# Optimization experiments

Measured on AMD Instinct MI355X. Metric: run time of the kernel, lower is better.

Reference implementation:

```python
import jax, jax.numpy as jnp
import numpy as np

HIDDEN = 1024
HEADS = 16
HEAD = HIDDEN // HEADS


def setup_inputs() -> dict:
    key = jax.random.key(0)
    ks = jax.random.split(key, 6)
    B, T = 2, 2048
    x = jax.random.normal(ks[0], (B, T, HIDDEN), dtype=jnp.float32)
    mask = jnp.ones((T, T), dtype=jnp.float32)
    s = 1.0 / np.sqrt(HIDDEN)
    Wqkv = jax.random.normal(ks[1], (HIDDEN, 3 * HIDDEN), dtype=jnp.float32) * s
    bqkv = jnp.zeros((3 * HIDDEN,), dtype=jnp.float32)
    Wproj = jax.random.normal(ks[2], (HIDDEN, HIDDEN), dtype=jnp.float32) * s
    bproj = jnp.zeros((HIDDEN,), dtype=jnp.float32)
    return {"x": x, "mask": mask, "Wqkv": Wqkv, "bqkv": bqkv,
            "Wproj": Wproj, "bproj": bproj}


def reference(x, mask, Wqkv, bqkv, Wproj, bproj):
    B, T, C = x.shape
    qkv = x @ Wqkv + bqkv                      # [B,T,3C]
    q, k, v = jnp.split(qkv, 3, axis=-1)
    def heads(t):                              # [B,T,C] -> [B,H,T,D]
        return t.reshape(B, T, HEADS, HEAD).transpose(0, 2, 1, 3)
    q, k, v = heads(q), heads(k), heads(v)
    scores = jnp.einsum('bhqd,bhkd->bhqk', q, k) / np.sqrt(HEAD)
    scores = jnp.where(mask == 0, -jnp.inf, scores)
    attn = jax.nn.softmax(scores, axis=-1)
    out = jnp.einsum('bhqk,bhkd->bhqd', attn, v)
    out = out.transpose(0, 2, 1, 3).reshape(B, T, C)
    return out @ Wproj + bproj
```

## Files before the change

kernel.cpp:

```cpp
#include <hip/hip_runtime.h>
#include <stdint.h>

#define HID 1024
#define NH 16
#define HD 64
#define BATCH 2
#define SEQ 2048
#define MR (BATCH*SEQ)
#define NQKV (3*HID)

typedef __attribute__((ext_vector_type(8))) _Float16 h16x8;
typedef __attribute__((ext_vector_type(4))) _Float16 h16x4;
typedef __attribute__((ext_vector_type(2))) __fp16 fp16x2;
typedef __attribute__((ext_vector_type(8))) unsigned short u16x8;
typedef __attribute__((ext_vector_type(4))) float f32x4;

#if __has_builtin(__builtin_amdgcn_exp2f)
#define EXP2(x) __builtin_amdgcn_exp2f(x)
#else
#define EXP2(x) exp2f(x)
#endif

static __device__ __forceinline__ unsigned short f2h(float f) {
  union { _Float16 h; unsigned short u; } v; v.h = (_Float16)f; return v.u;
}
static __device__ __forceinline__ unsigned pk2(float a, float b) {
  union { fp16x2 h; unsigned u; } v;
  v.h = __builtin_amdgcn_cvt_pkrtz(a, b);
  return v.u;
}

typedef const __attribute__((address_space(1))) unsigned int glb_u32;
typedef __attribute__((address_space(3))) unsigned int lds_u32;
static __device__ __forceinline__ void cp16(const void* g, void* l) {
  __builtin_amdgcn_global_load_lds((glb_u32*)g, (lds_u32*)l, 16, 0, 0);
}

#define QSCL (0.125f * 1.44269504f)

__global__ __launch_bounds__(256) void k_prep(const float4* __restrict__ x4,
                                              const float* __restrict__ mask,
                                              const float* __restrict__ Wqkv,
                                              const float* __restrict__ Wproj,
                                              ushort4* __restrict__ xh,
                                              unsigned short* __restrict__ WqT,
                                              unsigned short* __restrict__ WpT,
                                              unsigned long long* __restrict__ mb) {
  __shared__ float tile[32][33];
  int blk = blockIdx.x, tid = threadIdx.x;
  if (blk < 4096) {
    int i = blk * 256 + tid;
    float4 v = x4[i];
    ushort4 h;
    h.x = f2h(v.x); h.y = f2h(v.y); h.z = f2h(v.z); h.w = f2h(v.w);
    xh[i] = h;
  } else if (blk < 8192) {
    const float* src; unsigned short* dst; int C, bx, by;
    if (blk < 7168) { src = Wqkv;  dst = WqT; C = NQKV; int b2 = blk - 4096; bx = b2 % 96; by = b2 / 96; }
    else            { src = Wproj; dst = WpT; C = HID;  int b2 = blk - 7168; bx = b2 & 31; by = b2 >> 5; }
    int tx = tid & 31, ty = tid >> 5;
    int col0 = bx * 32, row0 = by * 32;
    #pragma unroll
    for (int i = 0; i < 32; i += 8)
      tile[ty + i][tx] = src[(size_t)(row0 + ty + i) * C + col0 + tx];
    __syncthreads();
    #pragma unroll
    for (int i = 0; i < 32; i += 8)
      dst[(size_t)(col0 + ty + i) * HID + row0 + tx] = f2h(tile[tx][ty + i]);
  } else {
    int gw = (blk - 8192) * 4 + (tid >> 6);
    int lane = tid & 63;
    float v = mask[(size_t)gw * 64 + lane];
    unsigned long long b = __ballot(v != 0.f);
    if (lane == 0) mb[gw] = b;
  }
}

__global__ __launch_bounds__(256) void k_gemm_qkv(const unsigned short* __restrict__ A,
                                                  const unsigned short* __restrict__ Bt,
                                                  const float* __restrict__ bias,
                                                  unsigned short* __restrict__ Qp,
                                                  unsigned short* __restrict__ Kp,
                                                  unsigned short* __restrict__ Vt) {
  const int K = HID;
  int tid = threadIdx.x;
  int wave = tid >> 6, lane = tid & 63, quad = lane >> 4, l16 = lane & 15;
  int wm = wave >> 1, wn = wave & 1;
  int x7 = l16 & 7;
  int m0 = blockIdx.y * 128, n0 = blockIdx.x * 128;
  __shared__ __align__(16) unsigned short smem[17408];
  unsigned short* As = smem;
  unsigned short* Bs = smem + 8192;
  unsigned short* Lb = smem;
  f32x4 acc[4][4] = {};
  for (int k0 = 0; k0 < K; k0 += 64) {
    __syncthreads();
    #pragma unroll
    for (int i = 0; i < 4; i++) {
      int c = tid + i * 256;
      int r = c >> 3, sc = ((c ^ r) & 7) << 3;
      cp16(&A[(size_t)(m0 + r) * K + k0 + sc], &As[c << 3]);
      cp16(&Bt[(size_t)(n0 + r) * K + k0 + sc], &Bs[c << 3]);
    }
    __syncthreads();
    #pragma unroll
    for (int kc = 0; kc < 2; kc++) {
      h16x8 af[4], bf[4];
      #pragma unroll
      for (int i = 0; i < 4; i++) {
        af[i] = *(const h16x8*)&As[(wm * 64 + i * 16 + l16) * 64 + (((kc * 4 + quad) ^ x7) << 3)];
        bf[i] = *(const h16x8*)&Bs[(wn * 64 + i * 16 + l16) * 64 + (((kc * 4 + quad) ^ x7) << 3)];
      }
      #pragma unroll
      for (int i = 0; i < 4; i++)
        #pragma unroll
        for (int j = 0; j < 4; j++)
          acc[i][j] = __builtin_amdgcn_mfma_f32_16x16x32_f16(af[i], bf[j], acc[i][j], 0, 0, 0);
    }
  }
  int which = n0 >> 10;
  int hbase = (n0 & 1023) >> 6;
  __syncthreads();
  if (which == 2) {
    #pragma unroll
    for (int j = 0; j < 4; j++) {
      int nl = wn * 64 + j * 16 + l16;
      float bv = bias[n0 + nl];
      #pragma unroll
      for (int i = 0; i < 4; i++) {
        int ml = wm * 64 + i * 16 + quad * 4;
        uint2 tt;
        tt.x = pk2(acc[i][j][0] + bv, acc[i][j][1] + bv);
        tt.y = pk2(acc[i][j][2] + bv, acc[i][j][3] + bv);
        *(uint2*)&Lb[nl * 136 + ml] = tt;
      }
    }
  } else {
    float scl = (which == 0) ? QSCL : 1.0f;
    #pragma unroll
    for (int j = 0; j < 4; j++) {
      int nl = wn * 64 + j * 16 + l16;
      float bv = bias[n0 + nl];
      #pragma unroll
      for (int i = 0; i < 4; i++)
        #pragma unroll
        for (int r = 0; r < 4; r++) {
          int ml = wm * 64 + i * 16 + quad * 4 + r;
          Lb[ml * 136 + nl] = f2h((acc[i][j][r] + bv) * scl);
        }
    }
  }
  __syncthreads();
  int b = m0 >> 11, tb = m0 & 2047;
  if (which == 2) {
    #pragma unroll
    for (int p = 0; p < 8; p++) {
      int c = tid + p * 256;
      int rr = c >> 4, cc = c & 15;
      int h = hbase + (rr >> 6), d = rr & 63;
      u16x8 vv = *(const u16x8*)&Lb[rr * 136 + cc * 8];
      *(u16x8*)&Vt[(size_t)(b * NH + h) * (SEQ * HD) + (size_t)d * SEQ + tb + cc * 8] = vv;
    }
  } else {
    unsigned short* dst = (which == 0) ? Qp : Kp;
    #pragma unroll
    for (int p = 0; p < 8; p++) {
      int c = tid + p * 256;
      int rr = c >> 4, cc = c & 15;
      int h = hbase + (cc >> 3), d0 = (cc & 7) << 3;
      u16x8 vv = *(const u16x8*)&Lb[rr * 136 + cc * 8];
      *(u16x8*)&dst[(size_t)(b * NH + h) * (SEQ * HD) + (size_t)(tb + rr) * HD + d0] = vv;
    }
  }
}

__global__ __launch_bounds__(256) void k_attn(const unsigned short* __restrict__ Qp,
                                              const unsigned short* __restrict__ Kp,
                                              const unsigned short* __restrict__ Vt,
                                              const unsigned long long* __restrict__ mb,
                                              unsigned short* __restrict__ AO) {
  int tid = threadIdx.x, wave = tid >> 6, lane = tid & 63, quad = lane >> 4, l16 = lane & 15;
  int bh = blockIdx.y, qbase = blockIdx.x * 128;
  const unsigned short* Qg = Qp + (size_t)bh * (SEQ * HD);
  const unsigned short* Kg = Kp + (size_t)bh * (SEQ * HD);
  const unsigned short* Vg = Vt + (size_t)bh * (SEQ * HD);
  __shared__ __align__(16) unsigned short smem[24576];
  unsigned short* Qs = smem;
  unsigned short* Os = smem;

  #pragma unroll
  for (int i = 0; i < 4; i++) {
    int c = tid + i * 256;
    int row = c >> 3, sc = ((c ^ row) & 7) << 3;
    cp16(&Qg[(size_t)(qbase + row) * HD + sc], &Qs[c << 3]);
  }
  #pragma unroll
  for (int i = 0; i < 2; i++) {
    int c = tid + i * 256;
    int row = c >> 3, sc = ((c ^ row) & 7) << 3;
    cp16(&Kg[(size_t)row * HD + sc], &smem[8192 + (c << 3)]);
    cp16(&Vg[(size_t)row * SEQ + sc], &smem[12288 + (c << 3)]);
  }
  int q0 = qbase + wave * 32 + l16;
  const unsigned long long* mrow0 = mb + (size_t)q0 * 32;
  const unsigned long long* mrow1 = mb + (size_t)(q0 + 16) * 32;
  f32x4 acc_o[2][4] = {};
  f32x4 acc_l[2] = {};
  int x7 = l16 & 7;

  h16x4 vone4;
  #pragma unroll
  for (int j = 0; j < 4; j++) vone4[j] = (_Float16)1.0f;

  __syncthreads();
  h16x8 bq[2][2];
  #pragma unroll
  for (int s = 0; s < 2; s++)
    #pragma unroll
    for (int kk = 0; kk < 2; kk++)
      bq[s][kk] = *(const h16x8*)&Qs[(wave * 32 + s * 16 + l16) * 64 + (((kk * 4 + quad) ^ x7) << 3)];

  for (int kt = 0; kt < 32; kt++) {
    unsigned short* cb = smem + 8192 + ((kt & 1) << 13);
    if (kt < 31) {
      unsigned short* nb = smem + 8192 + (((kt + 1) & 1) << 13);
      int kb2 = (kt + 1) * 64;
      #pragma unroll
      for (int i = 0; i < 2; i++) {
        int c = tid + i * 256;
        int row = c >> 3, sc = ((c ^ row) & 7) << 3;
        cp16(&Kg[(size_t)(kb2 + row) * HD + sc], &nb[c << 3]);
        cp16(&Vg[(size_t)row * SEQ + kb2 + sc], &nb[4096 + (c << 3)]);
      }
    }
    unsigned long long w0 = mrow0[kt], w1 = mrow1[kt];
    h16x8 ka[4][2];
    #pragma unroll
    for (int nt = 0; nt < 4; nt++)
      #pragma unroll
      for (int kk = 0; kk < 2; kk++)
        ka[nt][kk] = *(const h16x8*)&cb[(nt * 16 + l16) * 64 + (((kk * 4 + quad) ^ x7) << 3)];
    f32x4 s0[4] = {}, s1[4] = {};
    __builtin_amdgcn_s_setprio(1);
    #pragma unroll
    for (int nt = 0; nt < 4; nt++)
      #pragma unroll
      for (int kk = 0; kk < 2; kk++) {
        s0[nt] = __builtin_amdgcn_mfma_f32_16x16x32_f16(ka[nt][kk], bq[0][kk], s0[nt], 0, 0, 0);
        s1[nt] = __builtin_amdgcn_mfma_f32_16x16x32_f16(ka[nt][kk], bq[1][kk], s1[nt], 0, 0, 0);
      }
    __builtin_amdgcn_s_setprio(0);
    h16x4 va16[4][4];
    #pragma unroll
    for (int nt = 0; nt < 4; nt++)
      #pragma unroll
      for (int seg = 0; seg < 4; seg++)
        va16[nt][seg] = *(const h16x4*)&cb[4096 + (nt * 16 + l16) * 64 +
                                           (((seg * 2 + (quad >> 1)) ^ x7) << 3) +
                                           ((quad & 1) << 2)];
    if (!__all((w0 & w1) == ~0ULL)) {
      #pragma unroll
      for (int nt = 0; nt < 4; nt++)
        #pragma unroll
        for (int r = 0; r < 4; r++) {
          int bit = nt * 16 + quad * 4 + r;
          if (!((w0 >> bit) & 1ULL)) s0[nt][r] = -100.f;
          if (!((w1 >> bit) & 1ULL)) s1[nt][r] = -100.f;
        }
    }
    #pragma unroll
    for (int nt = 0; nt < 4; nt++)
      #pragma unroll
      for (int r = 0; r < 4; r++) {
        s0[nt][r] = EXP2(s0[nt][r]);
        s1[nt][r] = EXP2(s1[nt][r]);
      }
    auto pv = [&](const f32x4 (&s)[4], f32x4 (&ao)[4], f32x4 &al) {
      #pragma unroll
      for (int seg = 0; seg < 4; seg++) {
        union { h16x4 h; unsigned u[2]; } pb;
        pb.u[0] = pk2(s[seg][0], s[seg][1]);
        pb.u[1] = pk2(s[seg][2], s[seg][3]);
        al = __builtin_amdgcn_mfma_f32_16x16x16f16(vone4, pb.h, al, 0, 0, 0);
        #pragma unroll
        for (int nt = 0; nt < 4; nt++)
          ao[nt] = __builtin_amdgcn_mfma_f32_16x16x16f16(va16[nt][seg], pb.h, ao[nt], 0, 0, 0);
      }
    };
    __builtin_amdgcn_s_setprio(1);
    pv(s0, acc_o[0], acc_l[0]);
    pv(s1, acc_o[1], acc_l[1]);
    __builtin_amdgcn_s_setprio(0);
    asm volatile("s_waitcnt vmcnt(0)" ::: "memory");
    __builtin_amdgcn_s_barrier();
    __builtin_amdgcn_sched_barrier(0);
  }
  float rl0 = 1.0f / acc_l[0][0];
  float rl1 = 1.0f / acc_l[1][0];
  #pragma unroll
  for (int nt = 0; nt < 4; nt++) {
    uint2 t;
    t.x = (unsigned)f2h(acc_o[0][nt][0] * rl0) | ((unsigned)f2h(acc_o[0][nt][1] * rl0) << 16);
    t.y = (unsigned)f2h(acc_o[0][nt][2] * rl0) | ((unsigned)f2h(acc_o[0][nt][3] * rl0) << 16);
    *(uint2*)&Os[(wave * 32 + l16) * 72 + nt * 16 + quad * 4] = t;
    uint2 u;
    u.x = (unsigned)f2h(acc_o[1][nt][0] * rl1) | ((unsigned)f2h(acc_o[1][nt][1] * rl1) << 16);
    u.y = (unsigned)f2h(acc_o[1][nt][2] * rl1) | ((unsigned)f2h(acc_o[1][nt][3] * rl1) << 16);
    *(uint2*)&Os[(wave * 32 + 16 + l16) * 72 + nt * 16 + quad * 4] = u;
  }
  __syncthreads();
  int b = bh >> 4, h = bh & 15;
  #pragma unroll
  for (int i = 0; i < 4; i++) {
    int c = tid + i * 256;
    int row = c >> 3, co = (c & 7) << 3;
    u16x8 vv = *(const u16x8*)&Os[row * 72 + co];
    *(u16x8*)&AO[(size_t)(b * SEQ + qbase + row) * HID + h * HD + co] = vv;
  }
}

__global__ __launch_bounds__(256) void k_gemm_proj(const unsigned short* __restrict__ A,
                                                   const unsigned short* __restrict__ Bt,
                                                   const float* __restrict__ bias,
                                                   float* __restrict__ out) {
  const int K = HID;
  int tid = threadIdx.x;
  int wave = tid >> 6, lane = tid & 63, quad = lane >> 4, l16 = lane & 15;
  int wm = wave >> 1, wn = wave & 1;
  int x7 = l16 & 7;
  int m0 = blockIdx.y * 128, n0 = blockIdx.x * 64;
  __shared__ __align__(16) unsigned short smem[17408];
  unsigned short* As = smem;
  unsigned short* Bs = smem + 8192;
  float* Lf = (float*)smem;
  f32x4 acc[4][2] = {};
  for (int k0 = 0; k0 < K; k0 += 64) {
    __syncthreads();
    #pragma unroll
    for (int i = 0; i < 4; i++) {
      int c = tid + i * 256;
      int r = c >> 3, sc = ((c ^ r) & 7) << 3;
      cp16(&A[(size_t)(m0 + r) * K + k0 + sc], &As[c << 3]);
    }
    #pragma unroll
    for (int i = 0; i < 2; i++) {
      int c = tid + i * 256;
      int r = c >> 3, sc = ((c ^ r) & 7) << 3;
      cp16(&Bt[(size_t)(n0 + r) * K + k0 + sc], &Bs[c << 3]);
    }
    __syncthreads();
    #pragma unroll
    for (int kc = 0; kc < 2; kc++) {
      h16x8 af[4], bf[2];
      #pragma unroll
      for (int i = 0; i < 4; i++)
        af[i] = *(const h16x8*)&As[(wm * 64 + i * 16 + l16) * 64 + (((kc * 4 + quad) ^ x7) << 3)];
      #pragma unroll
      for (int j = 0; j < 2; j++)
        bf[j] = *(const h16x8*)&Bs[(wn * 32 + j * 16 + l16) * 64 + (((kc * 4 + quad) ^ x7) << 3)];
      #pragma unroll
      for (int i = 0; i < 4; i++)
        #pragma unroll
        for (int j = 0; j < 2; j++)
          acc[i][j] = __builtin_amdgcn_mfma_f32_16x16x32_f16(af[i], bf[j], acc[i][j], 0, 0, 0);
    }
  }
  __syncthreads();
  #pragma unroll
  for (int j = 0; j < 2; j++) {
    int nl = wn * 32 + j * 16 + l16;
    float bv = bias[n0 + nl];
    #pragma unroll
    for (int i = 0; i < 4; i++)
      #pragma unroll
      for (int r = 0; r < 4; r++) {
        int ml = wm * 64 + i * 16 + quad * 4 + r;
        Lf[ml * 68 + nl] = acc[i][j][r] + bv;
      }
  }
  __syncthreads();
  #pragma unroll
  for (int p = 0; p < 8; p++) {
    int c = tid + p * 256;
    int rr = c >> 4, cc = c & 15;
    float4 vv = *(const float4*)&Lf[rr * 68 + cc * 4];
    *(float4*)&out[(size_t)(m0 + rr) * HID + n0 + cc * 4] = vv;
  }
}

extern "C" void kernel_launch(void* const* d_in, const int* in_sizes, int n_in,
                              void* d_out, int out_size, void* d_ws, size_t ws_size,
                              hipStream_t stream) {
  const float* x     = (const float*)d_in[0];
  const float* mask  = (const float*)d_in[1];
  const float* Wqkv  = (const float*)d_in[2];
  const float* bqkv  = (const float*)d_in[3];
  const float* Wproj = (const float*)d_in[4];
  const float* bproj = (const float*)d_in[5];
  float* out = (float*)d_out;

  uint8_t* ws = (uint8_t*)d_ws;
  size_t off = 0;
  auto alloc = [&](size_t bytes) -> void* {
    void* p = (void*)(ws + off);
    off += (bytes + 255) & ~(size_t)255;
    return p;
  };
  unsigned short* xh   = (unsigned short*)alloc((size_t)MR * HID * 2);
  unsigned short* WqT  = (unsigned short*)alloc((size_t)NQKV * HID * 2);
  unsigned short* WpT  = (unsigned short*)alloc((size_t)HID * HID * 2);
  unsigned short* Qp   = (unsigned short*)alloc((size_t)BATCH * NH * SEQ * HD * 2);
  unsigned short* Kp   = (unsigned short*)alloc((size_t)BATCH * NH * SEQ * HD * 2);
  unsigned short* Vtp  = (unsigned short*)alloc((size_t)BATCH * NH * SEQ * HD * 2);
  unsigned short* AO   = (unsigned short*)alloc((size_t)MR * HID * 2);
  unsigned long long* mb = (unsigned long long*)alloc((size_t)SEQ * (SEQ / 64) * 8);

  k_prep<<<24576, 256, 0, stream>>>((const float4*)x, mask, Wqkv, Wproj,
                                    (ushort4*)xh, WqT, WpT, mb);
  k_gemm_qkv<<<dim3(NQKV / 128, MR / 128), 256, 0, stream>>>(xh, WqT, bqkv, Qp, Kp, Vtp);
  k_attn<<<dim3(SEQ / 128, BATCH * NH), 256, 0, stream>>>(Qp, Kp, Vtp, mb, AO);
  k_gemm_proj<<<dim3(HID / 64, MR / 128), 256, 0, stream>>>(AO, WpT, bproj, out);
}
```

Baseline: 207.1 us.

## Halve attention query tile to 64 rows and batch mask-packing per wave

The attention kernel now gives each block 64 query rows, one 16-row tile per wave instead of two, so twice as many blocks launch (1024 instead of 512) for better CU occupancy and fewer registers per thread. In exchange, every K/V tile is loaded from global memory twice as often across the grid, so K/V reuse per load is halved. Separately, the mask-prep path packs four 64-column words per wave instead of one, which halves the prep grid size and cuts per-block launch overhead.

After: 224.8 us. +8.5%, slower.

```diff
diff --git a/kernel.cpp b/kernel.cpp
--- a/kernel.cpp
+++ b/kernel.cpp
@@ -68,11 +68,15 @@
     for (int i = 0; i < 32; i += 8)
       dst[(size_t)(col0 + ty + i) * HID + row0 + tx] = f2h(tile[tx][ty + i]);
   } else {
-    int gw = (blk - 8192) * 4 + (tid >> 6);
+    int gw0 = (blk - 8192) * 16 + (tid >> 6) * 4;
     int lane = tid & 63;
-    float v = mask[(size_t)gw * 64 + lane];
-    unsigned long long b = __ballot(v != 0.f);
-    if (lane == 0) mb[gw] = b;
+    size_t base = (size_t)gw0 * 64;
+    #pragma unroll
+    for (int j = 0; j < 4; j++) {
+      float v = mask[base + j * 64 + lane];
+      unsigned long long b = __ballot(v != 0.f);
+      if (lane == 0) mb[gw0 + j] = b;
+    }
   }
 }
 
@@ -180,16 +184,16 @@
                                               const unsigned long long* __restrict__ mb,
                                               unsigned short* __restrict__ AO) {
   int tid = threadIdx.x, wave = tid >> 6, lane = tid & 63, quad = lane >> 4, l16 = lane & 15;
-  int bh = blockIdx.y, qbase = blockIdx.x * 128;
+  int bh = blockIdx.y, qbase = blockIdx.x * 64;
   const unsigned short* Qg = Qp + (size_t)bh * (SEQ * HD);
   const unsigned short* Kg = Kp + (size_t)bh * (SEQ * HD);
   const unsigned short* Vg = Vt + (size_t)bh * (SEQ * HD);
-  __shared__ __align__(16) unsigned short smem[24576];
+  __shared__ __align__(16) unsigned short smem[20480];
   unsigned short* Qs = smem;
   unsigned short* Os = smem;
 
   #pragma unroll
-  for (int i = 0; i < 4; i++) {
+  for (int i = 0; i < 2; i++) {
     int c = tid + i * 256;
     int row = c >> 3, sc = ((c ^ row) & 7) << 3;
     cp16(&Qg[(size_t)(qbase + row) * HD + sc], &Qs[c << 3]);
@@ -198,14 +202,13 @@
   for (int i = 0; i < 2; i++) {
     int c = tid + i * 256;
     int row = c >> 3, sc = ((c ^ row) & 7) << 3;
-    cp16(&Kg[(size_t)row * HD + sc], &smem[8192 + (c << 3)]);
-    cp16(&Vg[(size_t)row * SEQ + sc], &smem[12288 + (c << 3)]);
-  }
-  int q0 = qbase + wave * 32 + l16;
-  const unsigned long long* mrow0 = mb + (size_t)q0 * 32;
-  const unsigned long long* mrow1 = mb + (size_t)(q0 + 16) * 32;
-  f32x4 acc_o[2][4] = {};
-  f32x4 acc_l[2] = {};
+    cp16(&Kg[(size_t)row * HD + sc], &smem[4096 + (c << 3)]);
+    cp16(&Vg[(size_t)row * SEQ + sc], &smem[8192 + (c << 3)]);
+  }
+  int q0 = qbase + wave * 16 + l16;
+  const unsigned long long* mrow = mb + (size_t)q0 * 32;
+  f32x4 acc_o[4] = {};
+  f32x4 acc_l = {};
   int x7 = l16 & 7;
 
   h16x4 vone4;
@@ -213,17 +216,15 @@
   for (int j = 0; j < 4; j++) vone4[j] = (_Float16)1.0f;
 
   __syncthreads();
-  h16x8 bq[2][2];
-  #pragma unroll
-  for (int s = 0; s < 2; s++)
-    #pragma unroll
-    for (int kk = 0; kk < 2; kk++)
-      bq[s][kk] = *(const h16x8*)&Qs[(wave * 32 + s * 16 + l16) * 64 + (((kk * 4 + quad) ^ x7) << 3)];
+  h16x8 bq[2];
+  #pragma unroll
+  for (int kk = 0; kk < 2; kk++)
+    bq[kk] = *(const h16x8*)&Qs[(wave * 16 + l16) * 64 + (((kk * 4 + quad) ^ x7) << 3)];
 
   for (int kt = 0; kt < 32; kt++) {
-    unsigned short* cb = smem + 8192 + ((kt & 1) << 13);
+    unsigned short* cb = smem + 4096 + ((kt & 1) << 13);
     if (kt < 31) {
-      unsigned short* nb = smem + 8192 + (((kt + 1) & 1) << 13);
+      unsigned short* nb = smem + 4096 + (((kt + 1) & 1) << 13);
       int kb2 = (kt + 1) * 64;
       #pragma unroll
       for (int i = 0; i < 2; i++) {
@@ -233,22 +234,20 @@
         cp16(&Vg[(size_t)row * SEQ + kb2 + sc], &nb[4096 + (c << 3)]);
       }
     }
-    unsigned long long w0 = mrow0[kt], w1 = mrow1[kt];
+    unsigned long long w0 = mrow[kt];
     h16x8 ka[4][2];
     #pragma unroll
     for (int nt = 0; nt < 4; nt++)
       #pragma unroll
       for (int kk = 0; kk < 2; kk++)
         ka[nt][kk] = *(const h16x8*)&cb[(nt * 16 + l16) * 64 + (((kk * 4 + quad) ^ x7) << 3)];
-    f32x4 s0[4] = {}, s1[4] = {};
+    f32x4 s0[4] = {};
     __builtin_amdgcn_s_setprio(1);
     #pragma unroll
     for (int nt = 0; nt < 4; nt++)
       #pragma unroll
-      for (int kk = 0; kk < 2; kk++) {
-        s0[nt] = __builtin_amdgcn_mfma_f32_16x16x32_f16(ka[nt][kk], bq[0][kk], s0[nt], 0, 0, 0);
-        s1[nt] = __builtin_amdgcn_mfma_f32_16x16x32_f16(ka[nt][kk], bq[1][kk], s1[nt], 0, 0, 0);
-      }
+      for (int kk = 0; kk < 2; kk++)
+        s0[nt] = __builtin_amdgcn_mfma_f32_16x16x32_f16(ka[nt][kk], bq[kk], s0[nt], 0, 0, 0);
     __builtin_amdgcn_s_setprio(0);
     h16x4 va16[4][4];
     #pragma unroll
@@ -258,60 +257,48 @@
         va16[nt][seg] = *(const h16x4*)&cb[4096 + (nt * 16 + l16) * 64 +
                                            (((seg * 2 + (quad >> 1)) ^ x7) << 3) +
                                            ((quad & 1) << 2)];
-    if (!__all((w0 & w1) == ~0ULL)) {
+    if (!__all(w0 == ~0ULL)) {
       #pragma unroll
       for (int nt = 0; nt < 4; nt++)
         #pragma unroll
         for (int r = 0; r < 4; r++) {
           int bit = nt * 16 + quad * 4 + r;
           if (!((w0 >> bit) & 1ULL)) s0[nt][r] = -100.f;
-          if (!((w1 >> bit) & 1ULL)) s1[nt][r] = -100.f;
         }
     }
     #pragma unroll
     for (int nt = 0; nt < 4; nt++)
       #pragma unroll
-      for (int r = 0; r < 4; r++) {
+      for (int r = 0; r < 4; r++)
         s0[nt][r] = EXP2(s0[nt][r]);
-        s1[nt][r] = EXP2(s1[nt][r]);
-      }
-    auto pv = [&](const f32x4 (&s)[4], f32x4 (&ao)[4], f32x4 &al) {
-      #pragma unroll
-      for (int seg = 0; seg < 4; seg++) {
-        union { h16x4 h; unsigned u[2]; } pb;
-        pb.u[0] = pk2(s[seg][0], s[seg][1]);
-        pb.u[1] = pk2(s[seg][2], s[seg][3]);
-        al = __builtin_amdgcn_mfma_f32_16x16x16f16(vone4, pb.h, al, 0, 0, 0);
-        #pragma unroll
-        for (int nt = 0; nt < 4; nt++)
-          ao[nt] = __builtin_amdgcn_mfma_f32_16x16x16f16(va16[nt][seg], pb.h, ao[nt], 0, 0, 0);
-      }
-    };
     __builtin_amdgcn_s_setprio(1);
-    pv(s0, acc_o[0], acc_l[0]);
-    pv(s1, acc_o[1], acc_l[1]);
+    #pragma unroll
+    for (int seg = 0; seg < 4; seg++) {
+      union { h16x4 h; unsigned u[2]; } pb;
+      pb.u[0] = pk2(s0[seg][0], s0[seg][1]);
+      pb.u[1] = pk2(s0[seg][2], s0[seg][3]);
+      acc_l = __builtin_amdgcn_mfma_f32_16x16x16f16(vone4, pb.h, acc_l, 0, 0, 0);
+      #pragma unroll
+      for (int nt = 0; nt < 4; nt++)
+        acc_o[nt] = __builtin_amdgcn_mfma_f32_16x16x16f16(va16[nt][seg], pb.h, acc_o[nt], 0, 0, 0);
+    }
     __builtin_amdgcn_s_setprio(0);
     asm volatile("s_waitcnt vmcnt(0)" ::: "memory");
     __builtin_amdgcn_s_barrier();
     __builtin_amdgcn_sched_barrier(0);
   }
-  float rl0 = 1.0f / acc_l[0][0];
-  float rl1 = 1.0f / acc_l[1][0];
+  float rl = 1.0f / acc_l[0];
   #pragma unroll
   for (int nt = 0; nt < 4; nt++) {
     uint2 t;
-    t.x = (unsigned)f2h(acc_o[0][nt][0] * rl0) | ((unsigned)f2h(acc_o[0][nt][1] * rl0) << 16);
-    t.y = (unsigned)f2h(acc_o[0][nt][2] * rl0) | ((unsigned)f2h(acc_o[0][nt][3] * rl0) << 16);
-    *(uint2*)&Os[(wave * 32 + l16) * 72 + nt * 16 + quad * 4] = t;
-    uint2 u;
-    u.x = (unsigned)f2h(acc_o[1][nt][0] * rl1) | ((unsigned)f2h(acc_o[1][nt][1] * rl1) << 16);
-    u.y = (unsigned)f2h(acc_o[1][nt][2] * rl1) | ((unsigned)f2h(acc_o[1][nt][3] * rl1) << 16);
-    *(uint2*)&Os[(wave * 32 + 16 + l16) * 72 + nt * 16 + quad * 4] = u;
+    t.x = (unsigned)f2h(acc_o[nt][0] * rl) | ((unsigned)f2h(acc_o[nt][1] * rl) << 16);
+    t.y = (unsigned)f2h(acc_o[nt][2] * rl) | ((unsigned)f2h(acc_o[nt][3] * rl) << 16);
+    *(uint2*)&Os[(wave * 16 + l16) * 72 + nt * 16 + quad * 4] = t;
   }
   __syncthreads();
   int b = bh >> 4, h = bh & 15;
   #pragma unroll
-  for (int i = 0; i < 4; i++) {
+  for (int i = 0; i < 2; i++) {
     int c = tid + i * 256;
     int row = c >> 3, co = (c & 7) << 3;
     u16x8 vv = *(const u16x8*)&Os[row * 72 + co];
@@ -415,9 +402,9 @@
   unsigned short* AO   = (unsigned short*)alloc((size_t)MR * HID * 2);
   unsigned long long* mb = (unsigned long long*)alloc((size_t)SEQ * (SEQ / 64) * 8);
 
-  k_prep<<<24576, 256, 0, stream>>>((const float4*)x, mask, Wqkv, Wproj,
+  k_prep<<<12288, 256, 0, stream>>>((const float4*)x, mask, Wqkv, Wproj,
                                     (ushort4*)xh, WqT, WpT, mb);
   k_gemm_qkv<<<dim3(NQKV / 128, MR / 128), 256, 0, stream>>>(xh, WqT, bqkv, Qp, Kp, Vtp);
-  k_attn<<<dim3(SEQ / 128, BATCH * NH), 256, 0, stream>>>(Qp, Kp, Vtp, mb, AO);
+  k_attn<<<dim3(SEQ / 64, BATCH * NH), 256, 0, stream>>>(Qp, Kp, Vtp, mb, AO);
   k_gemm_proj<<<dim3(HID / 64, MR / 128), 256, 0, stream>>>(AO, WpT, bproj, out);
 }
```
